# Kernel optimization log

Hardware: AMD Instinct MI355X
Metric: run time of the kernel (lower is better)

The kernel has to match this reference:

```python
import jax, jax.numpy as jnp
import numpy as np

KH, KW = 3, 3
STRIDE = 1
OUT_C = 512


def im2col(x, kh, kw, stride):
    # x: [N, C, H, W] -> col: [C*kh*kw, N*oh*ow]  (row order: C major, then kh, kw)
    N, C, H, W = x.shape
    oh = (H - kh) // stride + 1
    ow = (W - kw) // stride + 1
    rows = jnp.arange(oh)[:, None] * stride + jnp.arange(kh)[None, :]  # [oh, kh]
    cols = jnp.arange(ow)[:, None] * stride + jnp.arange(kw)[None, :]  # [ow, kw]
    # gather windows: result [N, C, oh, kh, ow, kw]
    A = x[:, :, rows[:, :, None, None], cols[None, None, :, :]]
    # permute to (C, kh, kw, N, oh, ow) then flatten, matching torch permute(1,4,5,0,2,3)
    col = jnp.transpose(A, (1, 3, 5, 0, 2, 4)).reshape(C * kh * kw, N * oh * ow)
    return col, oh, ow


def setup_inputs() -> dict:
    key = jax.random.key(0)
    k1, k2, k3 = jax.random.split(key, 3)
    N, C, H, W = 16, 256, 32, 32
    K_sel = (C * KH * KW) // 2  # 1152 rows kept by the binary mask
    x = jax.random.normal(k1, (N, C, H, W), dtype=jnp.float32)
    weight = jax.random.normal(k2, (K_sel, OUT_C), dtype=jnp.float32) * 0.02
    idx = jnp.sort(jax.random.randint(k3, (K_sel,), 0, C * KH * KW, dtype=jnp.int32))
    return {"x": x, "weight": weight, "idx": idx}


def reference(x, weight, idx):
    N = x.shape[0]
    col, oh, ow = im2col(x, KH, KW, STRIDE)          # [C*kh*kw, N*oh*ow]
    x_tile = col[idx, :].T                            # gather masked rows -> [N*oh*ow, K_sel]
    conv_out = x_tile @ weight                        # [N*oh*ow, out_c]
    conv_out = conv_out.reshape(N, oh * ow, OUT_C)
    conv_out = jnp.transpose(conv_out, (0, 2, 1)).reshape(N, OUT_C, oh, ow)
    return conv_out
```

## Files before the change

kernel.cpp:

```cpp
#include <hip/hip_runtime.h>
#include <stdint.h>

#define N_IMG   16
#define C_IN    256
#define H_IN    32
#define W_IN    32
#define OH      30
#define OW      30
#define K_SEL   1152
#define OUTC    512
#define RY_TOT  (N_IMG * OH)
#define M_HAT   (RY_TOT * 32)
#define X_ELEMS (N_IMG * C_IN * H_IN * W_IN)
#define OUT_SP  (OH * OW)

typedef float f32x4  __attribute__((ext_vector_type(4)));
typedef short bf16x8 __attribute__((ext_vector_type(8)));

__device__ __forceinline__ unsigned short f2bf(float f) {
    unsigned int u = __float_as_uint(f);
    u += 0x7FFFu + ((u >> 16) & 1u);
    return (unsigned short)(u >> 16);
}

__device__ __forceinline__ void gl_lds16(const void* g, void* lds) {
    __builtin_amdgcn_global_load_lds(
        (const __attribute__((address_space(1))) unsigned int*)g,
        (__attribute__((address_space(3))) unsigned int*)lds,
        16, 0, 0);
}

__global__ void koff_kernel(const int* __restrict__ idx, int* __restrict__ koff) {
    int k = blockIdx.x * 256 + threadIdx.x;
    if (k < K_SEL) {
        int v   = idx[k];
        int c   = v / 9;
        int rem = v - c * 9;
        int i   = rem / 3;
        int j   = rem - i * 3;
        koff[k] = c * (H_IN * W_IN) + i * W_IN + j;
    }
}

__global__ void wt_kernel(const float* __restrict__ w, unsigned short* __restrict__ wT) {
    int id = blockIdx.x * 256 + threadIdx.x;
    int o  = id / K_SEL;
    int s  = id - o * K_SEL;
    wT[id] = f2bf(w[s * OUTC + o]);
}

__global__ void amat_kernel(const float* __restrict__ x, const int* __restrict__ koff,
                            unsigned short* __restrict__ Am) {
    __shared__ float tile[32 * 129];
    const int rb = blockIdx.x;
    const int kb = blockIdx.y;
    const int t  = threadIdx.x;
    const int n  = rb / OH;
    const int y  = rb - n * OH;
    const int base = n * (C_IN * H_IN * W_IN) + y * W_IN;

    const int xw = t & 31;
    const int kq = t >> 5;
#pragma unroll
    for (int r = 0; r < 16; ++r) {
        int kl = kq * 16 + r;
        int g  = base + koff[kb * 128 + kl] + xw;
        g = min(g, X_ELEMS - 1);
        tile[xw * 129 + kl] = x[g];
    }
    __syncthreads();

    const int kp = t & 63;
    const int xg = t >> 6;
#pragma unroll
    for (int r = 0; r < 8; ++r) {
        int xw2 = r * 4 + xg;
        float f0 = tile[xw2 * 129 + 2 * kp];
        float f1 = tile[xw2 * 129 + 2 * kp + 1];
        unsigned int pk = (unsigned int)f2bf(f0) | ((unsigned int)f2bf(f1) << 16);
        size_t off = (size_t)(rb * 32 + xw2) * K_SEL + kb * 128 + 2 * kp;
        *reinterpret_cast<unsigned int*>(&Am[off]) = pk;
    }
}

__global__ __launch_bounds__(256) void gemm_kernel(const unsigned short* __restrict__ wT,
                                                   const unsigned short* __restrict__ Am,
                                                   float* __restrict__ out) {
    __shared__ __align__(16) unsigned short As[128 * 32];
    __shared__ __align__(16) unsigned short Bs[128 * 32];

    const int t    = threadIdx.x;
    const int wave = t >> 6;
    const int lane = t & 63;
    const int quad = lane >> 4;
    const int lo   = lane & 15;

    const int ot = blockIdx.x & 3;
    const int mt = blockIdx.x >> 2;
    const int oBase = ot * 128;
    const int mBase = mt * 128;
    const int wo = (wave & 1) * 64;
    const int wm = (wave >> 1) * 64;

    f32x4 acc[4][4] = {};

    const int lrow = lane >> 2;
    const int lks  = (lane & 3) * 8;
    const unsigned short* wrow0 = wT + (size_t)(oBase + wave * 16 + lrow) * K_SEL + lks;
    const unsigned short* wrow1 = wrow0 + (size_t)64 * K_SEL;
    const unsigned short* arow0 = Am + (size_t)(mBase + wave * 16 + lrow) * K_SEL + lks;
    const unsigned short* arow1 = arow0 + (size_t)64 * K_SEL;
    unsigned short* lA0 = &As[(wave * 16) * 32];
    unsigned short* lA1 = &As[(64 + wave * 16) * 32];
    unsigned short* lB0 = &Bs[(wave * 16) * 32];
    unsigned short* lB1 = &Bs[(64 + wave * 16) * 32];

    for (int kt = 0; kt < K_SEL / 32; ++kt) {
        const int k0 = kt * 32;
        gl_lds16(wrow0 + k0, lA0);
        gl_lds16(wrow1 + k0, lA1);
        gl_lds16(arow0 + k0, lB0);
        gl_lds16(arow1 + k0, lB1);
        __syncthreads();

        bf16x8 a[4], b[4];
#pragma unroll
        for (int ms = 0; ms < 4; ++ms)
            a[ms] = *(const bf16x8*)&As[(wo + ms * 16 + lo) * 32 + quad * 8];
#pragma unroll
        for (int ns = 0; ns < 4; ++ns)
            b[ns] = *(const bf16x8*)&Bs[(wm + ns * 16 + lo) * 32 + quad * 8];
#pragma unroll
        for (int ms = 0; ms < 4; ++ms)
#pragma unroll
            for (int ns = 0; ns < 4; ++ns)
                acc[ms][ns] = __builtin_amdgcn_mfma_f32_16x16x32_bf16(
                    a[ms], b[ns], acc[ms][ns], 0, 0, 0);
        __syncthreads();
    }

#pragma unroll
    for (int ns = 0; ns < 4; ++ns) {
        const int mh = mBase + wm + ns * 16 + lo;
        const int xw = mh & 31;
        const unsigned int ry = (unsigned int)(mh >> 5);
        const unsigned int n  = ry / 30u;
        const unsigned int yy = ry - n * 30u;
        if (xw < OW) {
            const size_t ob = (size_t)n * (OUTC * OUT_SP) + (size_t)yy * OW + xw;
#pragma unroll
            for (int ms = 0; ms < 4; ++ms) {
                const int o0 = oBase + wo + ms * 16 + quad * 4;
#pragma unroll
                for (int r = 0; r < 4; ++r)
                    out[ob + (size_t)(o0 + r) * OUT_SP] = acc[ms][ns][r];
            }
        }
    }
}

extern "C" void kernel_launch(void* const* d_in, const int* in_sizes, int n_in,
                              void* d_out, int out_size, void* d_ws, size_t ws_size,
                              hipStream_t stream) {
    const float* x   = (const float*)d_in[0];
    const float* w   = (const float*)d_in[1];
    const int*   idx = (const int*)d_in[2];
    float*       out = (float*)d_out;

    char* ws = (char*)d_ws;
    int*            koff = (int*)ws;
    unsigned short* wT   = (unsigned short*)(ws + 4608);
    unsigned short* Am   = (unsigned short*)(ws + 4608 + 1179648);

    koff_kernel<<<dim3(5), dim3(256), 0, stream>>>(idx, koff);
    wt_kernel<<<dim3((OUTC * K_SEL) / 256), dim3(256), 0, stream>>>(w, wT);
    amat_kernel<<<dim3(RY_TOT, K_SEL / 128), dim3(256), 0, stream>>>(x, koff, Am);
    gemm_kernel<<<dim3((M_HAT / 128) * (OUTC / 128)), dim3(256), 0, stream>>>(wT, Am, out);
}
```

Baseline: 123.6 us.

## Split GEMM K dimension in two with partial buffers and combine kernel

Splits the GEMM reduction over K into two halves, doubling the block count from 480 to 960. Each half writes fp32 partial results to a workspace buffer, and a new combine kernel sums them into the NCHW output. The prep kernels for koff and the weight transpose are also merged into one launch. The aim is better CU occupancy on the 256-CU device, paid for with extra partial writes and reads of about 2x31MB and one more kernel launch.

Result: slower. 138.8 us (+12.3%).

```diff
diff --git a/kernel.cpp b/kernel.cpp
--- a/kernel.cpp
+++ b/kernel.cpp
@@ -13,6 +13,8 @@
 #define M_HAT   (RY_TOT * 32)
 #define X_ELEMS (N_IMG * C_IN * H_IN * W_IN)
 #define OUT_SP  (OH * OW)
+#define NSPLIT  2
+#define KITERS  (K_SEL / 32 / NSPLIT)
 
 typedef float f32x4  __attribute__((ext_vector_type(4)));
 typedef short bf16x8 __attribute__((ext_vector_type(8)));
@@ -30,22 +32,19 @@
         16, 0, 0);
 }
 
-__global__ void koff_kernel(const int* __restrict__ idx, int* __restrict__ koff) {
-    int k = blockIdx.x * 256 + threadIdx.x;
-    if (k < K_SEL) {
-        int v   = idx[k];
+__global__ void prep_kernel(const int* __restrict__ idx, const float* __restrict__ w,
+                            int* __restrict__ koff, unsigned short* __restrict__ wT) {
+    int id = blockIdx.x * 256 + threadIdx.x;
+    if (id < K_SEL) {
+        int v   = idx[id];
         int c   = v / 9;
         int rem = v - c * 9;
         int i   = rem / 3;
         int j   = rem - i * 3;
-        koff[k] = c * (H_IN * W_IN) + i * W_IN + j;
+        koff[id] = c * (H_IN * W_IN) + i * W_IN + j;
     }
-}
-
-__global__ void wt_kernel(const float* __restrict__ w, unsigned short* __restrict__ wT) {
-    int id = blockIdx.x * 256 + threadIdx.x;
-    int o  = id / K_SEL;
-    int s  = id - o * K_SEL;
+    int o = id / K_SEL;
+    int s = id - o * K_SEL;
     wT[id] = f2bf(w[s * OUTC + o]);
 }
 
@@ -85,7 +84,7 @@
 
 __global__ __launch_bounds__(256) void gemm_kernel(const unsigned short* __restrict__ wT,
                                                    const unsigned short* __restrict__ Am,
-                                                   float* __restrict__ out) {
+                                                   float* __restrict__ partial) {
     __shared__ __align__(16) unsigned short As[128 * 32];
     __shared__ __align__(16) unsigned short Bs[128 * 32];
 
@@ -95,8 +94,10 @@
     const int quad = lane >> 4;
     const int lo   = lane & 15;
 
-    const int ot = blockIdx.x & 3;
-    const int mt = blockIdx.x >> 2;
+    const int bid = blockIdx.x;
+    const int sp = bid & 1;
+    const int ot = (bid >> 1) & 3;
+    const int mt = bid >> 3;
     const int oBase = ot * 128;
     const int mBase = mt * 128;
     const int wo = (wave & 1) * 64;
@@ -115,7 +116,8 @@
     unsigned short* lB0 = &Bs[(wave * 16) * 32];
     unsigned short* lB1 = &Bs[(64 + wave * 16) * 32];
 
-    for (int kt = 0; kt < K_SEL / 32; ++kt) {
+    const int ktBeg = sp * KITERS;
+    for (int kt = ktBeg; kt < ktBeg + KITERS; ++kt) {
         const int k0 = kt * 32;
         gl_lds16(wrow0 + k0, lA0);
         gl_lds16(wrow1 + k0, lA1);
@@ -139,24 +141,30 @@
         __syncthreads();
     }
 
+    float* pbase = partial + (size_t)sp * OUTC * M_HAT;
 #pragma unroll
     for (int ns = 0; ns < 4; ++ns) {
         const int mh = mBase + wm + ns * 16 + lo;
-        const int xw = mh & 31;
-        const unsigned int ry = (unsigned int)(mh >> 5);
-        const unsigned int n  = ry / 30u;
-        const unsigned int yy = ry - n * 30u;
-        if (xw < OW) {
-            const size_t ob = (size_t)n * (OUTC * OUT_SP) + (size_t)yy * OW + xw;
 #pragma unroll
-            for (int ms = 0; ms < 4; ++ms) {
-                const int o0 = oBase + wo + ms * 16 + quad * 4;
+        for (int ms = 0; ms < 4; ++ms) {
+            const int o0 = oBase + wo + ms * 16 + quad * 4;
 #pragma unroll
-                for (int r = 0; r < 4; ++r)
-                    out[ob + (size_t)(o0 + r) * OUT_SP] = acc[ms][ns][r];
-            }
+            for (int r = 0; r < 4; ++r)
+                pbase[(size_t)(o0 + r) * M_HAT + mh] = acc[ms][ns][r];
         }
     }
+}
+
+__global__ void combine_kernel(const float* __restrict__ p, float* __restrict__ out) {
+    int id = blockIdx.x * 256 + threadIdx.x;
+    int n = id / (OUTC * OUT_SP);
+    int r = id - n * (OUTC * OUT_SP);
+    int o = r / OUT_SP;
+    int s = r - o * OUT_SP;
+    int y = s / OW;
+    int xw = s - y * OW;
+    size_t i0 = (size_t)o * M_HAT + (size_t)((n * OH + y) * 32 + xw);
+    out[id] = p[i0] + p[(size_t)OUTC * M_HAT + i0];
 }
 
 extern "C" void kernel_launch(void* const* d_in, const int* in_sizes, int n_in,
@@ -171,9 +179,10 @@
     int*            koff = (int*)ws;
     unsigned short* wT   = (unsigned short*)(ws + 4608);
     unsigned short* Am   = (unsigned short*)(ws + 4608 + 1179648);
+    float*          part = (float*)(ws + 4608 + 1179648 + 35389440);
 
-    koff_kernel<<<dim3(5), dim3(256), 0, stream>>>(idx, koff);
-    wt_kernel<<<dim3((OUTC * K_SEL) / 256), dim3(256), 0, stream>>>(w, wT);
+    prep_kernel<<<dim3((OUTC * K_SEL) / 256), dim3(256), 0, stream>>>(idx, w, koff, wT);
     amat_kernel<<<dim3(RY_TOT, K_SEL / 128), dim3(256), 0, stream>>>(x, koff, Am);
-    gemm_kernel<<<dim3((M_HAT / 128) * (OUTC / 128)), dim3(256), 0, stream>>>(wT, Am, out);
+    gemm_kernel<<<dim3((M_HAT / 128) * (OUTC / 128) * NSPLIT), dim3(256), 0, stream>>>(wT, Am, part);
+    combine_kernel<<<dim3((N_IMG * OUTC * OUT_SP) / 256), dim3(256), 0, stream>>>(part, out);
 }
```

## Fuse im2col gather into GEMM and merge weight prep kernels

Applied to the files above, without the earlier changes.

Removes the separate im2col materialization kernel. The GEMM now gathers x values through koff held in shared memory, converts them to bf16 and writes them into LDS, with a register double-buffered prefetch of the next K step. koff and weight-transpose prep are merged into one kernel, and the weight transpose now goes through an LDS tile for coalescing. The GEMM tile shrinks to 128x64 with launch bounds for more occupancy, which saves the Am round trip through memory at the cost of uncoalesced-ish scalar gathers inside the GEMM loop and more blocks re-reading x.

Result: faster. 113.5 us (-8.2%).

```diff
diff --git a/kernel.cpp b/kernel.cpp
--- a/kernel.cpp
+++ b/kernel.cpp
@@ -13,6 +13,14 @@
 #define M_HAT   (RY_TOT * 32)
 #define X_ELEMS (N_IMG * C_IN * H_IN * W_IN)
 #define OUT_SP  (OH * OW)
+#define CHW     (C_IN * H_IN * W_IN)
+
+#define TO      128
+#define TM      64
+#define NMT     (M_HAT / TM)
+#define NOT     (OUTC / TO)
+#define BSTR    40
+#define KITER   (K_SEL / 32)
 
 typedef float f32x4  __attribute__((ext_vector_type(4)));
 typedef short bf16x8 __attribute__((ext_vector_type(8)));
@@ -30,64 +38,43 @@
         16, 0, 0);
 }
 
-__global__ void koff_kernel(const int* __restrict__ idx, int* __restrict__ koff) {
-    int k = blockIdx.x * 256 + threadIdx.x;
-    if (k < K_SEL) {
-        int v   = idx[k];
-        int c   = v / 9;
-        int rem = v - c * 9;
-        int i   = rem / 3;
-        int j   = rem - i * 3;
-        koff[k] = c * (H_IN * W_IN) + i * W_IN + j;
-    }
-}
-
-__global__ void wt_kernel(const float* __restrict__ w, unsigned short* __restrict__ wT) {
-    int id = blockIdx.x * 256 + threadIdx.x;
-    int o  = id / K_SEL;
-    int s  = id - o * K_SEL;
-    wT[id] = f2bf(w[s * OUTC + o]);
-}
-
-__global__ void amat_kernel(const float* __restrict__ x, const int* __restrict__ koff,
-                            unsigned short* __restrict__ Am) {
-    __shared__ float tile[32 * 129];
-    const int rb = blockIdx.x;
-    const int kb = blockIdx.y;
-    const int t  = threadIdx.x;
-    const int n  = rb / OH;
-    const int y  = rb - n * OH;
-    const int base = n * (C_IN * H_IN * W_IN) + y * W_IN;
-
-    const int xw = t & 31;
-    const int kq = t >> 5;
-#pragma unroll
-    for (int r = 0; r < 16; ++r) {
-        int kl = kq * 16 + r;
-        int g  = base + koff[kb * 128 + kl] + xw;
-        g = min(g, X_ELEMS - 1);
-        tile[xw * 129 + kl] = x[g];
+__global__ void prep_kernel(const int* __restrict__ idx, const float* __restrict__ w,
+                            int* __restrict__ koff, unsigned short* __restrict__ wT) {
+    __shared__ float tile[32][33];
+    const int bx = blockIdx.x, by = blockIdx.y, t = threadIdx.x;
+
+    if (by == 0) {
+        int k = bx * 256 + t;
+        if (k < K_SEL) {
+            int v = idx[k];
+            int c = v / 9, rem = v - c * 9;
+            int i = rem / 3, j = rem - i * 3;
+            koff[k] = c * (H_IN * W_IN) + i * W_IN + j;
+        }
+    }
+    const int s0 = bx * 32, o0 = by * 32;
+    const int oc = t & 31, sg = t >> 5;
+#pragma unroll
+    for (int i = 0; i < 4; ++i) {
+        int sl = sg * 4 + i;
+        tile[sl][oc] = w[(s0 + sl) * OUTC + o0 + oc];
     }
     __syncthreads();
-
-    const int kp = t & 63;
-    const int xg = t >> 6;
-#pragma unroll
-    for (int r = 0; r < 8; ++r) {
-        int xw2 = r * 4 + xg;
-        float f0 = tile[xw2 * 129 + 2 * kp];
-        float f1 = tile[xw2 * 129 + 2 * kp + 1];
-        unsigned int pk = (unsigned int)f2bf(f0) | ((unsigned int)f2bf(f1) << 16);
-        size_t off = (size_t)(rb * 32 + xw2) * K_SEL + kb * 128 + 2 * kp;
-        *reinterpret_cast<unsigned int*>(&Am[off]) = pk;
-    }
-}
-
-__global__ __launch_bounds__(256) void gemm_kernel(const unsigned short* __restrict__ wT,
-                                                   const unsigned short* __restrict__ Am,
-                                                   float* __restrict__ out) {
-    __shared__ __align__(16) unsigned short As[128 * 32];
-    __shared__ __align__(16) unsigned short Bs[128 * 32];
+    const int ol = t >> 3, sq = t & 7;
+    unsigned int u0 = (unsigned int)f2bf(tile[sq * 4 + 0][ol]) |
+                      ((unsigned int)f2bf(tile[sq * 4 + 1][ol]) << 16);
+    unsigned int u1 = (unsigned int)f2bf(tile[sq * 4 + 2][ol]) |
+                      ((unsigned int)f2bf(tile[sq * 4 + 3][ol]) << 16);
+    uint2 pk; pk.x = u0; pk.y = u1;
+    *reinterpret_cast<uint2*>(&wT[(size_t)(o0 + ol) * K_SEL + s0 + sq * 4]) = pk;
+}
+
+__global__ __launch_bounds__(256, 4)
+void gemm_kernel(const unsigned short* __restrict__ wT, const float* __restrict__ x,
+                 const int* __restrict__ koff, float* __restrict__ out) {
+    __shared__ __align__(16) unsigned short As[TO * 32];
+    __shared__ __align__(16) unsigned short Bs[TM * BSTR];
+    __shared__ int koS[K_SEL];
 
     const int t    = threadIdx.x;
     const int wave = t >> 6;
@@ -95,43 +82,88 @@
     const int quad = lane >> 4;
     const int lo   = lane & 15;
 
-    const int ot = blockIdx.x & 3;
-    const int mt = blockIdx.x >> 2;
-    const int oBase = ot * 128;
-    const int mBase = mt * 128;
-    const int wo = (wave & 1) * 64;
-    const int wm = (wave >> 1) * 64;
-
-    f32x4 acc[4][4] = {};
-
-    const int lrow = lane >> 2;
-    const int lks  = (lane & 3) * 8;
-    const unsigned short* wrow0 = wT + (size_t)(oBase + wave * 16 + lrow) * K_SEL + lks;
-    const unsigned short* wrow1 = wrow0 + (size_t)64 * K_SEL;
-    const unsigned short* arow0 = Am + (size_t)(mBase + wave * 16 + lrow) * K_SEL + lks;
-    const unsigned short* arow1 = arow0 + (size_t)64 * K_SEL;
-    unsigned short* lA0 = &As[(wave * 16) * 32];
-    unsigned short* lA1 = &As[(64 + wave * 16) * 32];
-    unsigned short* lB0 = &Bs[(wave * 16) * 32];
-    unsigned short* lB1 = &Bs[(64 + wave * 16) * 32];
-
-    for (int kt = 0; kt < K_SEL / 32; ++kt) {
+    const int bid = blockIdx.x;
+    const int mt  = bid % NMT;
+    const int ot  = bid / NMT;
+    const int oBase = ot * TO;
+    const int mBase = mt * TM;
+
+    for (int i = t; i < K_SEL; i += 256) koS[i] = koff[i];
+
+    int base[2];
+#pragma unroll
+    for (int ry = 0; ry < 2; ++ry) {
+        int ryg = mt * 2 + ry;
+        int n = ryg / 30, y = ryg - n * 30;
+        base[ry] = n * CHW + y * W_IN;
+    }
+
+    const int xw  = t & 31;
+    const int kq4 = t >> 5;
+    const int ks  = kq4 * 4;
+
+    const int lrow = lane >> 2, lks = (lane & 3) * 8;
+    const unsigned short* wrow0 = wT + (size_t)(oBase + wave * 32 + lrow) * K_SEL + lks;
+    const unsigned short* wrow1 = wrow0 + (size_t)16 * K_SEL;
+    unsigned short* lA0 = &As[(wave * 32) * 32];
+    unsigned short* lA1 = lA0 + 16 * 32;
+
+    __syncthreads();
+
+    f32x4 acc[2][4] = {};
+    int   kk[2][4];
+    float v[2][2][4];
+
+#pragma unroll
+    for (int j = 0; j < 4; ++j) kk[0][j] = koS[ks + j];
+#pragma unroll
+    for (int ry = 0; ry < 2; ++ry)
+#pragma unroll
+        for (int j = 0; j < 4; ++j) {
+            int g = base[ry] + kk[0][j] + xw;
+            g = min(g, X_ELEMS - 1);
+            v[0][ry][j] = x[g];
+        }
+
+#pragma unroll 2
+    for (int kt = 0; kt < KITER; ++kt) {
+        const int p = kt & 1, q = p ^ 1;
         const int k0 = kt * 32;
         gl_lds16(wrow0 + k0, lA0);
         gl_lds16(wrow1 + k0, lA1);
-        gl_lds16(arow0 + k0, lB0);
-        gl_lds16(arow1 + k0, lB1);
+#pragma unroll
+        for (int ry = 0; ry < 2; ++ry) {
+            unsigned int u0 = (unsigned int)f2bf(v[p][ry][0]) |
+                              ((unsigned int)f2bf(v[p][ry][1]) << 16);
+            unsigned int u1 = (unsigned int)f2bf(v[p][ry][2]) |
+                              ((unsigned int)f2bf(v[p][ry][3]) << 16);
+            uint2 pk; pk.x = u0; pk.y = u1;
+            *reinterpret_cast<uint2*>(&Bs[(ry * 32 + xw) * BSTR + ks]) = pk;
+        }
+        if (kt + 1 < KITER) {
+            const int k1 = k0 + 32;
+#pragma unroll
+            for (int j = 0; j < 4; ++j) kk[q][j] = koS[k1 + ks + j];
+#pragma unroll
+            for (int ry = 0; ry < 2; ++ry)
+#pragma unroll
+                for (int j = 0; j < 4; ++j) {
+                    int g = base[ry] + kk[q][j] + xw;
+                    g = min(g, X_ELEMS - 1);
+                    v[q][ry][j] = x[g];
+                }
+        }
         __syncthreads();
 
-        bf16x8 a[4], b[4];
-#pragma unroll
-        for (int ms = 0; ms < 4; ++ms)
-            a[ms] = *(const bf16x8*)&As[(wo + ms * 16 + lo) * 32 + quad * 8];
+        bf16x8 a[2], b[4];
+#pragma unroll
+        for (int ms = 0; ms < 2; ++ms)
+            a[ms] = *(const bf16x8*)&As[(wave * 32 + ms * 16 + lo) * 32 + quad * 8];
 #pragma unroll
         for (int ns = 0; ns < 4; ++ns)
-            b[ns] = *(const bf16x8*)&Bs[(wm + ns * 16 + lo) * 32 + quad * 8];
-#pragma unroll
-        for (int ms = 0; ms < 4; ++ms)
+            b[ns] = *(const bf16x8*)&Bs[(ns * 16 + lo) * BSTR + quad * 8];
+#pragma unroll
+        for (int ms = 0; ms < 2; ++ms)
 #pragma unroll
             for (int ns = 0; ns < 4; ++ns)
                 acc[ms][ns] = __builtin_amdgcn_mfma_f32_16x16x32_bf16(
@@ -141,16 +173,15 @@
 
 #pragma unroll
     for (int ns = 0; ns < 4; ++ns) {
-        const int mh = mBase + wm + ns * 16 + lo;
-        const int xw = mh & 31;
-        const unsigned int ry = (unsigned int)(mh >> 5);
-        const unsigned int n  = ry / 30u;
-        const unsigned int yy = ry - n * 30u;
-        if (xw < OW) {
-            const size_t ob = (size_t)n * (OUTC * OUT_SP) + (size_t)yy * OW + xw;
-#pragma unroll
-            for (int ms = 0; ms < 4; ++ms) {
-                const int o0 = oBase + wo + ms * 16 + quad * 4;
+        const int mh  = mBase + ns * 16 + lo;
+        const int xwe = mh & 31;
+        const int ryg = mh >> 5;
+        const int n = ryg / 30, y = ryg - n * 30;
+        if (xwe < OW) {
+            const size_t ob = (size_t)n * (OUTC * OUT_SP) + (size_t)y * OW + xwe;
+#pragma unroll
+            for (int ms = 0; ms < 2; ++ms) {
+                const int o0 = oBase + wave * 32 + ms * 16 + quad * 4;
 #pragma unroll
                 for (int r = 0; r < 4; ++r)
                     out[ob + (size_t)(o0 + r) * OUT_SP] = acc[ms][ns][r];
@@ -170,10 +201,7 @@
     char* ws = (char*)d_ws;
     int*            koff = (int*)ws;
     unsigned short* wT   = (unsigned short*)(ws + 4608);
-    unsigned short* Am   = (unsigned short*)(ws + 4608 + 1179648);
-
-    koff_kernel<<<dim3(5), dim3(256), 0, stream>>>(idx, koff);
-    wt_kernel<<<dim3((OUTC * K_SEL) / 256), dim3(256), 0, stream>>>(w, wT);
-    amat_kernel<<<dim3(RY_TOT, K_SEL / 128), dim3(256), 0, stream>>>(x, koff, Am);
-    gemm_kernel<<<dim3((M_HAT / 128) * (OUTC / 128)), dim3(256), 0, stream>>>(wT, Am, out);
-}
+
+    prep_kernel<<<dim3(K_SEL / 32, OUTC / 32), dim3(256), 0, stream>>>(idx, w, koff, wT);
+    gemm_kernel<<<dim3(NMT * NOT), dim3(256), 0, stream>>>(wT, x, koff, out);
+}
```
